# Performance work log

Measured on AMD Instinct MI355X. Metric: run time of the kernel, lower is better.

Reference implementation:

```python
import jax, jax.numpy as jnp
import numpy as np

# Fixed reactor dimensions and grey-box constants (from hyb_greybox_pars / xuyscales)
NX, NU, NY, NP = 3, 1, 2, 4
NZ = NP * (NY + NU)          # 12
F, V, DELTA = 0.1, 1.0, 1.0
CAMEAN, CBMEAN = 1.0, 0.5    # yscale mean
CASTD, CBSTD = 0.5, 0.3      # yscale std
CAFMEAN, CAFSTD = 2.0, 0.5   # uscale


def _fnn(x, layers):
    """Feed-forward NN: tanh hidden layers, linear output layer."""
    for W, b in layers[:-1]:
        x = jnp.tanh(x @ W + b)
    W, b = layers[-1]
    return x @ W + b


def setup_inputs() -> dict:
    key = jax.random.key(0)
    ks = jax.random.split(key, 16)
    B, T = 2048, 1024
    d = {
        "useq": jax.random.normal(ks[0], (B, T, NU), jnp.float32),
        "x0": 0.1 * jax.random.normal(ks[1], (B, NX + NZ), jnp.float32),
    }
    s1 = 1.0 / np.sqrt(1.0)
    s16 = 1.0 / np.sqrt(16.0)
    s12 = 1.0 / np.sqrt(12.0)
    s32 = 1.0 / np.sqrt(32.0)
    for i, name in enumerate(["r1", "r2", "r3"]):
        d[name + "_W0"] = s1 * jax.random.normal(ks[2 + 2 * i], (1, 16), jnp.float32)
        d[name + "_b0"] = jnp.zeros((16,), jnp.float32)
        d[name + "_W1"] = s16 * jax.random.normal(ks[3 + 2 * i], (16, 1), jnp.float32)
        d[name + "_b1"] = jnp.zeros((1,), jnp.float32)
    d["estC_W0"] = s12 * jax.random.normal(ks[10], (12, 32), jnp.float32)
    d["estC_b0"] = jnp.zeros((32,), jnp.float32)
    d["estC_W1"] = s32 * jax.random.normal(ks[11], (32, 1), jnp.float32)
    d["estC_b1"] = jnp.zeros((1,), jnp.float32)
    return d


def reference(useq, x0,
              r1_W0, r1_b0, r1_W1, r1_b1,
              r2_W0, r2_b0, r2_W1, r2_b1,
              r3_W0, r3_b0, r3_W1, r3_b1,
              estC_W0, estC_b0, estC_W1, estC_b1):
    r1L = [(r1_W0, r1_b0), (r1_W1, r1_b1)]
    r2L = [(r2_W0, r2_b0), (r2_W1, r2_b1)]
    r3L = [(r3_W0, r3_b0), (r3_W1, r3_b1)]
    estCL = [(estC_W0, estC_b0), (estC_W1, estC_b1)]

    def fxu(x, u):
        Ca, Cb, Cc = x[:, 0:1], x[:, 1:2], x[:, 2:3]
        Caf = u[:, 0:1]
        r1 = _fnn(Ca, r1L) * CASTD
        r2 = _fnn(Cb, r2L) * CBSTD
        r3 = _fnn(Cc, r3L) * CBSTD
        Ca = Ca * CASTD + CAMEAN
        Cb = Cb * CBSTD + CBMEAN
        Cc = Cc * CBSTD + CBMEAN
        Caf = Caf * CAFSTD + CAFMEAN
        dCa = F * (Caf - Ca) / V - r1
        dCb = -F * Cb / V + r1 - 3.0 * r2 + r3
        dCc = -F * Cc / V + r2 - r3
        return jnp.concatenate([dCa / CASTD, dCb / CBSTD, dCc / CBSTD], axis=-1)

    def step(xz, u):
        x, z = xz[:, :NX], xz[:, NX:]
        ypseq, upseq = z[:, :NP * NY], z[:, NP * NY:]
        k1 = fxu(x, u)
        k2 = fxu(x + DELTA * (k1 / 2.0), u)
        k3 = fxu(x + DELTA * (k2 / 2.0), u)
        k4 = fxu(x + DELTA * k3, u)
        xplus = x + (DELTA / 6.0) * (k1 + 2.0 * k2 + 2.0 * k3 + k4)
        zplus = jnp.concatenate([ypseq[:, NY:], x[:, :NY], upseq[:, NU:], u], axis=-1)
        CcNN = _fnn(z, estCL)
        y = jnp.concatenate([x, CcNN], axis=-1)   # [B, Ny + 2*numUnmeasGb] = [B, 4]
        return jnp.concatenate([xplus, zplus], axis=-1), y

    u_t = jnp.swapaxes(useq, 0, 1)                # [T, B, Nu]
    _, ys = jax.lax.scan(step, x0, u_t)           # ys: [T, B, 4]
    return jnp.swapaxes(ys, 0, 1)                 # [B, T, 4]
```

## Files before the change

### kernel.cpp

```cpp
#include <hip/hip_runtime.h>

#define TT 1024
#define BB 2048
#define K1 8
#define L2E2 2.8853900817779268f

typedef float v2f __attribute__((ext_vector_type(2)));

template <int CTRL>
__device__ __forceinline__ float dpp_add(float x) {
  int y = __builtin_amdgcn_update_dpp(0, __float_as_int(x), CTRL, 0xF, 0xF, true);
  return x + __int_as_float(y);
}
__device__ __forceinline__ float sum16(float x) {
  x = dpp_add<0xB1>(x);
  x = dpp_add<0x4E>(x);
  x = dpp_add<0x141>(x);
  x = dpp_add<0x140>(x);
  return x;
}
__device__ __forceinline__ float rdlane(float x, int l) {
  return __int_as_float(__builtin_amdgcn_readlane(__float_as_int(x), l));
}
__device__ __forceinline__ v2f pkfma(float s, v2f w, v2f a) {
  return __builtin_elementwise_fma((v2f){s, s}, w, a);
}

__global__ __launch_bounds__(256) void phase1_kernel(
    const float* __restrict__ useq, const float* __restrict__ x0,
    const float* __restrict__ r1W0, const float* __restrict__ r1b0,
    const float* __restrict__ r1W1, const float* __restrict__ r1b1,
    const float* __restrict__ r2W0, const float* __restrict__ r2b0,
    const float* __restrict__ r2W1, const float* __restrict__ r2b1,
    const float* __restrict__ r3W0, const float* __restrict__ r3b0,
    const float* __restrict__ r3W1, const float* __restrict__ r3b1,
    float* __restrict__ out) {
  const int lane = threadIdx.x & 63;
  const int row = lane >> 4;
  const int j = lane & 15;
  const int e =
      __builtin_amdgcn_readfirstlane(blockIdx.x * 4 + (threadIdx.x >> 6));

  const float* W0p = (row == 0) ? r1W0 : (row == 1) ? r2W0 : r3W0;
  const float* b0p = (row == 0) ? r1b0 : (row == 1) ? r2b0 : r3b0;
  const float* W1p = (row == 0) ? r1W1 : (row == 1) ? r2W1 : r3W1;

  const float w0s = W0p[j] * L2E2;
  const float b0s = b0p[j] * L2E2;
  const float wn = -2.0f * W1p[j];
  const float iwn = 1.0f / wn;

  float C1 = r1b1[0], C2 = r2b1[0], C3 = r3b1[0];
  for (int q = 0; q < 16; ++q) {
    C1 += r1W1[q];
    C2 += r2W1[q];
    C3 += r3W1[q];
  }
  const float caC = 0.2f - C1;
  const float cbC = -1.0f / 6.0f + (5.0f / 3.0f) * C1 - 3.0f * C2 + C3;
  const float ccC = -1.0f / 6.0f + C2 - C3;

  const float cstBase = (row == 0) ? caC : (row == 1) ? cbC : ccC;
  const float uco = (row == 0) ? 0.1f : 0.0f;
  const float a1 = (row == 0) ? -1.0f : (row == 1) ? (5.0f / 3.0f) : 0.0f;
  const float a2 = (row == 1) ? -3.0f : (row == 2) ? 1.0f : 0.0f;
  const float a3 = (row == 1) ? 1.0f : (row == 2) ? -1.0f : 0.0f;

  float S = x0[e * 15 + ((row < 3) ? row : 2)];

  const float* up = useq + e * TT;
  float* op = out + (size_t)e * TT * 4;

#define STAGE(SS, KK)                                                     \
  {                                                                       \
    float e_ = __builtin_amdgcn_exp2f(fmaf(w0s, (SS), b0s));              \
    float q = sum16(__builtin_amdgcn_rcpf(fmaf(e_, iwn, iwn)));           \
    float P1 = rdlane(q, 0);                                              \
    float P2 = rdlane(q, 16);                                             \
    float P3 = rdlane(q, 32);                                             \
    float t_ = fmaf(-0.1f, (SS), cstS);                                   \
    t_ = fmaf(a1, P1, t_);                                                \
    t_ = fmaf(a2, P2, t_);                                                \
    KK = fmaf(a3, P3, t_);                                                \
  }

#define STEP(UQ, SC_)                                                     \
  {                                                                       \
    const float cstS = fmaf(uco, (UQ), cstBase);                          \
    SC_ = S;                                                              \
    float k1, k2, k3, k4;                                                 \
    STAGE(S, k1)                                                          \
    float s2 = fmaf(0.5f, k1, S);                                         \
    STAGE(s2, k2)                                                         \
    float s3 = fmaf(0.5f, k2, S);                                         \
    STAGE(s3, k3)                                                         \
    float s4 = S + k3;                                                    \
    STAGE(s4, k4)                                                         \
    S = fmaf(1.0f / 6.0f, fmaf(2.0f, k2 + k3, k1) + k4, S);               \
  }

  float uc0, uc1, uc2, uc3, uc4, uc5, uc6, uc7;
  {
    float4 a = *(const float4*)(up);
    float4 b = *(const float4*)(up + 4);
    uc0 = a.x; uc1 = a.y; uc2 = a.z; uc3 = a.w;
    uc4 = b.x; uc5 = b.y; uc6 = b.z; uc7 = b.w;
  }

  for (int t0 = 0; t0 < TT; t0 += K1) {
    const int tn = (t0 + K1 <= TT - K1) ? (t0 + K1) : (TT - K1);
    const float4 na = *(const float4*)(up + tn);
    const float4 nb = *(const float4*)(up + tn + 4);

    float sc0, sc1, sc2, sc3, sc4, sc5, sc6, sc7;
    STEP(uc0, sc0)
    STEP(uc1, sc1)
    STEP(uc2, sc2)
    STEP(uc3, sc3)
    STEP(uc4, sc4)
    STEP(uc5, sc5)
    STEP(uc6, sc6)
    STEP(uc7, sc7)

    if (j == 0 && row < 3) {
      float* p = op + t0 * 4 + row;
      p[0] = sc0;  p[4] = sc1;  p[8] = sc2;  p[12] = sc3;
      p[16] = sc4; p[20] = sc5; p[24] = sc6; p[28] = sc7;
    }

    uc0 = na.x; uc1 = na.y; uc2 = na.z; uc3 = na.w;
    uc4 = nb.x; uc5 = nb.y; uc6 = nb.z; uc7 = nb.w;
  }
#undef STEP
#undef STAGE
}

__global__ __launch_bounds__(256) void phase2_kernel(
    const float* __restrict__ useq, const float* __restrict__ x0,
    const float* __restrict__ W0, const float* __restrict__ b0,
    const float* __restrict__ W1, const float* __restrict__ b1p,
    float* __restrict__ out) {
  __shared__ float4 wq[16][8];
  if (threadIdx.x < 128) {
    const int p = threadIdx.x >> 3, q = threadIdx.x & 7;
    float4 v = {0.0f, 0.0f, 0.0f, 0.0f};
    if (q < 6) {
      v.x = W0[(2 * q) * 32 + 2 * p] * L2E2;
      v.y = W0[(2 * q) * 32 + 2 * p + 1] * L2E2;
      v.z = W0[(2 * q + 1) * 32 + 2 * p] * L2E2;
      v.w = W0[(2 * q + 1) * 32 + 2 * p + 1] * L2E2;
    } else if (q == 6) {
      v.x = b0[2 * p] * L2E2;
      v.y = b0[2 * p + 1] * L2E2;
      v.z = -2.0f * W1[2 * p];
      v.w = -2.0f * W1[2 * p + 1];
    }
    wq[p][q] = v;
  }
  __syncthreads();

  float base = b1p[0];
#pragma unroll
  for (int h = 0; h < 32; ++h) base += W1[h];

  const int b = blockIdx.x * 2 + (threadIdx.x >> 7);
  const int tid = threadIdx.x & 127;
  const float* xrow = x0 + b * 15;

  v2f zy[8][4];
  float zu[8][4];
#pragma unroll
  for (int k = 0; k < 8; ++k) {
    const int t = k * 128 + tid;
    const int g = (b << 10) + t;
    if (t >= 4) {
      const v2f* py = (const v2f*)(out) + (size_t)(g - 4) * 2;
#pragma unroll
      for (int i = 0; i < 4; ++i) zy[k][i] = py[2 * i];
      const float* pu = useq + g - 4;
#pragma unroll
      for (int i = 0; i < 4; ++i) zu[k][i] = pu[i];
    } else {
#pragma unroll
      for (int i = 0; i < 4; ++i) {
        const int s4 = t - 4 + i;
        if (s4 >= 0) {
          const v2f* py = (const v2f*)(out) + (size_t)((b << 10) + s4) * 2;
          zy[k][i] = py[0];
          zu[k][i] = useq[(b << 10) + s4];
        } else {
          zy[k][i] = (v2f){xrow[3 + 2 * (i + t)], xrow[4 + 2 * (i + t)]};
          zu[k][i] = xrow[11 + i + t];
        }
      }
    }
  }

  float ov0 = base, ov1 = base, ov2 = base, ov3 = base;
  float ov4 = base, ov5 = base, ov6 = base, ov7 = base;
#pragma unroll
  for (int p = 0; p < 16; ++p) {
    const float4 w01 = wq[p][0];
    const float4 w23 = wq[p][1];
    const float4 w45 = wq[p][2];
    const float4 w67 = wq[p][3];
    const float4 wu01 = wq[p][4];
    const float4 wu23 = wq[p][5];
    const float4 wb = wq[p][6];
#define ACC2(OV, ZY, ZU)                                                  \
  {                                                                       \
    v2f a = (v2f){wb.x, wb.y};                                            \
    a = pkfma(ZY[0].x, (v2f){w01.x, w01.y}, a);                           \
    a = pkfma(ZY[0].y, (v2f){w01.z, w01.w}, a);                           \
    a = pkfma(ZY[1].x, (v2f){w23.x, w23.y}, a);                           \
    a = pkfma(ZY[1].y, (v2f){w23.z, w23.w}, a);                           \
    a = pkfma(ZY[2].x, (v2f){w45.x, w45.y}, a);                           \
    a = pkfma(ZY[2].y, (v2f){w45.z, w45.w}, a);                           \
    a = pkfma(ZY[3].x, (v2f){w67.x, w67.y}, a);                           \
    a = pkfma(ZY[3].y, (v2f){w67.z, w67.w}, a);                           \
    a = pkfma(ZU[0], (v2f){wu01.x, wu01.y}, a);                           \
    a = pkfma(ZU[1], (v2f){wu01.z, wu01.w}, a);                           \
    a = pkfma(ZU[2], (v2f){wu23.x, wu23.y}, a);                           \
    a = pkfma(ZU[3], (v2f){wu23.z, wu23.w}, a);                           \
    const float sx =                                                      \
        __builtin_amdgcn_rcpf(__builtin_amdgcn_exp2f(a.x) + 1.0f);        \
    const float sy =                                                      \
        __builtin_amdgcn_rcpf(__builtin_amdgcn_exp2f(a.y) + 1.0f);        \
    OV = fmaf(wb.z, sx, OV);                                              \
    OV = fmaf(wb.w, sy, OV);                                              \
  }
    ACC2(ov0, zy[0], zu[0])
    ACC2(ov1, zy[1], zu[1])
    ACC2(ov2, zy[2], zu[2])
    ACC2(ov3, zy[3], zu[3])
    ACC2(ov4, zy[4], zu[4])
    ACC2(ov5, zy[5], zu[5])
    ACC2(ov6, zy[6], zu[6])
    ACC2(ov7, zy[7], zu[7])
#undef ACC2
  }

  const size_t gb = (size_t)(b << 10) + tid;
  out[(gb + 0) * 4 + 3] = ov0;
  out[(gb + 128) * 4 + 3] = ov1;
  out[(gb + 256) * 4 + 3] = ov2;
  out[(gb + 384) * 4 + 3] = ov3;
  out[(gb + 512) * 4 + 3] = ov4;
  out[(gb + 640) * 4 + 3] = ov5;
  out[(gb + 768) * 4 + 3] = ov6;
  out[(gb + 896) * 4 + 3] = ov7;
}

extern "C" void kernel_launch(void* const* d_in, const int* in_sizes, int n_in,
                              void* d_out, int out_size, void* d_ws,
                              size_t ws_size, hipStream_t stream) {
  const float* useq = (const float*)d_in[0];
  const float* x0 = (const float*)d_in[1];
  float* out = (float*)d_out;

  phase1_kernel<<<BB / 4, 256, 0, stream>>>(
      useq, x0,
      (const float*)d_in[2], (const float*)d_in[3], (const float*)d_in[4],
      (const float*)d_in[5], (const float*)d_in[6], (const float*)d_in[7],
      (const float*)d_in[8], (const float*)d_in[9], (const float*)d_in[10],
      (const float*)d_in[11], (const float*)d_in[12], (const float*)d_in[13],
      out);

  phase2_kernel<<<BB / 2, 256, 0, stream>>>(
      useq, x0, (const float*)d_in[14], (const float*)d_in[15],
      (const float*)d_in[16], (const float*)d_in[17], out);
}
```

Baseline: 445.0 us.

## Interleave two batch trajectories per wave in RK4 scan; contiguous time windows in phase2

Phase 1 now has each wavefront integrate two independent batch rows at once, interleaving their exp/rcp/DPP-reduction/readlane chains. The aim is to hide the long serial dependency latency of the per-step recurrence, at the cost of launching half as many blocks. Phase 2 now gives each thread 8 consecutive timesteps and builds them from a shared 11-element sliding window, instead of gathering 4-wide history separately for strided timesteps, which cuts redundant global loads. The lower block count in phase 1 may reduce occupancy across CUs.

```diff
diff --git a/kernel.cpp b/kernel.cpp
--- a/kernel.cpp
+++ b/kernel.cpp
@@ -2,7 +2,6 @@
 
 #define TT 1024
 #define BB 2048
-#define K1 8
 #define L2E2 2.8853900817779268f
 
 typedef float v2f __attribute__((ext_vector_type(2)));
@@ -11,13 +10,6 @@
 __device__ __forceinline__ float dpp_add(float x) {
   int y = __builtin_amdgcn_update_dpp(0, __float_as_int(x), CTRL, 0xF, 0xF, true);
   return x + __int_as_float(y);
-}
-__device__ __forceinline__ float sum16(float x) {
-  x = dpp_add<0xB1>(x);
-  x = dpp_add<0x4E>(x);
-  x = dpp_add<0x141>(x);
-  x = dpp_add<0x140>(x);
-  return x;
 }
 __device__ __forceinline__ float rdlane(float x, int l) {
   return __int_as_float(__builtin_amdgcn_readlane(__float_as_int(x), l));
@@ -38,8 +30,9 @@
   const int lane = threadIdx.x & 63;
   const int row = lane >> 4;
   const int j = lane & 15;
-  const int e =
-      __builtin_amdgcn_readfirstlane(blockIdx.x * 4 + (threadIdx.x >> 6));
+  const int e0 = __builtin_amdgcn_readfirstlane(
+      (blockIdx.x * 4 + (threadIdx.x >> 6)) * 2);
+  const int e1 = e0 + 1;
 
   const float* W0p = (row == 0) ? r1W0 : (row == 1) ? r2W0 : r3W0;
   const float* b0p = (row == 0) ? r1b0 : (row == 1) ? r2b0 : r3b0;
@@ -66,73 +59,81 @@
   const float a2 = (row == 1) ? -3.0f : (row == 2) ? 1.0f : 0.0f;
   const float a3 = (row == 1) ? 1.0f : (row == 2) ? -1.0f : 0.0f;
 
-  float S = x0[e * 15 + ((row < 3) ? row : 2)];
-
-  const float* up = useq + e * TT;
-  float* op = out + (size_t)e * TT * 4;
-
-#define STAGE(SS, KK)                                                     \
+  const int srow = (row < 3) ? row : 2;
+  float S0 = x0[e0 * 15 + srow];
+  float S1 = x0[e1 * 15 + srow];
+
+  const float* up0 = useq + e0 * TT;
+  const float* up1 = useq + e1 * TT;
+  float* op0 = out + (size_t)e0 * TT * 4;
+  float* op1 = out + (size_t)e1 * TT * 4;
+
+#define STAGE2(SA, SB, KA, KB)                                            \
   {                                                                       \
-    float e_ = __builtin_amdgcn_exp2f(fmaf(w0s, (SS), b0s));              \
-    float q = sum16(__builtin_amdgcn_rcpf(fmaf(e_, iwn, iwn)));           \
-    float P1 = rdlane(q, 0);                                              \
-    float P2 = rdlane(q, 16);                                             \
-    float P3 = rdlane(q, 32);                                             \
-    float t_ = fmaf(-0.1f, (SS), cstS);                                   \
-    t_ = fmaf(a1, P1, t_);                                                \
-    t_ = fmaf(a2, P2, t_);                                                \
-    KK = fmaf(a3, P3, t_);                                                \
-  }
-
-#define STEP(UQ, SC_)                                                     \
+    float ea_ = __builtin_amdgcn_exp2f(fmaf(w0s, (SA), b0s));             \
+    float eb_ = __builtin_amdgcn_exp2f(fmaf(w0s, (SB), b0s));             \
+    float qa_ = __builtin_amdgcn_rcpf(fmaf(ea_, iwn, iwn));               \
+    float qb_ = __builtin_amdgcn_rcpf(fmaf(eb_, iwn, iwn));               \
+    qa_ = dpp_add<0xB1>(qa_);   qb_ = dpp_add<0xB1>(qb_);                 \
+    qa_ = dpp_add<0x4E>(qa_);   qb_ = dpp_add<0x4E>(qb_);                 \
+    qa_ = dpp_add<0x141>(qa_);  qb_ = dpp_add<0x141>(qb_);                \
+    qa_ = dpp_add<0x140>(qa_);  qb_ = dpp_add<0x140>(qb_);                \
+    float P1a = rdlane(qa_, 0);                                           \
+    float P1b = rdlane(qb_, 0);                                           \
+    float P2a = rdlane(qa_, 16);                                          \
+    float P2b = rdlane(qb_, 16);                                          \
+    float P3a = rdlane(qa_, 32);                                          \
+    float P3b = rdlane(qb_, 32);                                          \
+    float ta_ = fmaf(-0.1f, (SA), cstSa);                                 \
+    float tb_ = fmaf(-0.1f, (SB), cstSb);                                 \
+    ta_ = fmaf(a1, P1a, ta_);   tb_ = fmaf(a1, P1b, tb_);                 \
+    ta_ = fmaf(a2, P2a, ta_);   tb_ = fmaf(a2, P2b, tb_);                 \
+    KA = fmaf(a3, P3a, ta_);    KB = fmaf(a3, P3b, tb_);                  \
+  }
+
+#define STEP2(UA, UB, SCA, SCB)                                           \
   {                                                                       \
-    const float cstS = fmaf(uco, (UQ), cstBase);                          \
-    SC_ = S;                                                              \
-    float k1, k2, k3, k4;                                                 \
-    STAGE(S, k1)                                                          \
-    float s2 = fmaf(0.5f, k1, S);                                         \
-    STAGE(s2, k2)                                                         \
-    float s3 = fmaf(0.5f, k2, S);                                         \
-    STAGE(s3, k3)                                                         \
-    float s4 = S + k3;                                                    \
-    STAGE(s4, k4)                                                         \
-    S = fmaf(1.0f / 6.0f, fmaf(2.0f, k2 + k3, k1) + k4, S);               \
-  }
-
-  float uc0, uc1, uc2, uc3, uc4, uc5, uc6, uc7;
-  {
-    float4 a = *(const float4*)(up);
-    float4 b = *(const float4*)(up + 4);
-    uc0 = a.x; uc1 = a.y; uc2 = a.z; uc3 = a.w;
-    uc4 = b.x; uc5 = b.y; uc6 = b.z; uc7 = b.w;
-  }
-
-  for (int t0 = 0; t0 < TT; t0 += K1) {
-    const int tn = (t0 + K1 <= TT - K1) ? (t0 + K1) : (TT - K1);
-    const float4 na = *(const float4*)(up + tn);
-    const float4 nb = *(const float4*)(up + tn + 4);
-
-    float sc0, sc1, sc2, sc3, sc4, sc5, sc6, sc7;
-    STEP(uc0, sc0)
-    STEP(uc1, sc1)
-    STEP(uc2, sc2)
-    STEP(uc3, sc3)
-    STEP(uc4, sc4)
-    STEP(uc5, sc5)
-    STEP(uc6, sc6)
-    STEP(uc7, sc7)
+    const float cstSa = fmaf(uco, (UA), cstBase);                         \
+    const float cstSb = fmaf(uco, (UB), cstBase);                         \
+    SCA = S0;  SCB = S1;                                                  \
+    float k1a, k2a, k3a, k4a, k1b, k2b, k3b, k4b;                         \
+    STAGE2(S0, S1, k1a, k1b)                                              \
+    float s2a = fmaf(0.5f, k1a, S0), s2b = fmaf(0.5f, k1b, S1);           \
+    STAGE2(s2a, s2b, k2a, k2b)                                            \
+    float s3a = fmaf(0.5f, k2a, S0), s3b = fmaf(0.5f, k2b, S1);           \
+    STAGE2(s3a, s3b, k3a, k3b)                                            \
+    float s4a = S0 + k3a, s4b = S1 + k3b;                                 \
+    STAGE2(s4a, s4b, k4a, k4b)                                            \
+    S0 = fmaf(1.0f / 6.0f, fmaf(2.0f, k2a + k3a, k1a) + k4a, S0);         \
+    S1 = fmaf(1.0f / 6.0f, fmaf(2.0f, k2b + k3b, k1b) + k4b, S1);         \
+  }
+
+  float4 cura = *(const float4*)(up0);
+  float4 curb = *(const float4*)(up1);
+
+  for (int t0 = 0; t0 < TT; t0 += 4) {
+    const int tn = (t0 + 4 <= TT - 4) ? (t0 + 4) : (TT - 4);
+    const float4 naa = *(const float4*)(up0 + tn);
+    const float4 nab = *(const float4*)(up1 + tn);
+
+    float sa0, sa1, sa2, sa3, sb0, sb1, sb2, sb3;
+    STEP2(cura.x, curb.x, sa0, sb0)
+    STEP2(cura.y, curb.y, sa1, sb1)
+    STEP2(cura.z, curb.z, sa2, sb2)
+    STEP2(cura.w, curb.w, sa3, sb3)
 
     if (j == 0 && row < 3) {
-      float* p = op + t0 * 4 + row;
-      p[0] = sc0;  p[4] = sc1;  p[8] = sc2;  p[12] = sc3;
-      p[16] = sc4; p[20] = sc5; p[24] = sc6; p[28] = sc7;
-    }
-
-    uc0 = na.x; uc1 = na.y; uc2 = na.z; uc3 = na.w;
-    uc4 = nb.x; uc5 = nb.y; uc6 = nb.z; uc7 = nb.w;
-  }
-#undef STEP
-#undef STAGE
+      float* pa = op0 + t0 * 4 + row;
+      pa[0] = sa0;  pa[4] = sa1;  pa[8] = sa2;  pa[12] = sa3;
+      float* pb = op1 + t0 * 4 + row;
+      pb[0] = sb0;  pb[4] = sb1;  pb[8] = sb2;  pb[12] = sb3;
+    }
+
+    cura = naa;
+    curb = nab;
+  }
+#undef STEP2
+#undef STAGE2
 }
 
 __global__ __launch_bounds__(256) void phase2_kernel(
@@ -165,39 +166,41 @@
 
   const int b = blockIdx.x * 2 + (threadIdx.x >> 7);
   const int tid = threadIdx.x & 127;
+  const int t0 = tid * 8;
   const float* xrow = x0 + b * 15;
 
-  v2f zy[8][4];
-  float zu[8][4];
-#pragma unroll
-  for (int k = 0; k < 8; ++k) {
-    const int t = k * 128 + tid;
-    const int g = (b << 10) + t;
-    if (t >= 4) {
-      const v2f* py = (const v2f*)(out) + (size_t)(g - 4) * 2;
-#pragma unroll
-      for (int i = 0; i < 4; ++i) zy[k][i] = py[2 * i];
-      const float* pu = useq + g - 4;
-#pragma unroll
-      for (int i = 0; i < 4; ++i) zu[k][i] = pu[i];
-    } else {
-#pragma unroll
-      for (int i = 0; i < 4; ++i) {
-        const int s4 = t - 4 + i;
-        if (s4 >= 0) {
-          const v2f* py = (const v2f*)(out) + (size_t)((b << 10) + s4) * 2;
-          zy[k][i] = py[0];
-          zu[k][i] = useq[(b << 10) + s4];
-        } else {
-          zy[k][i] = (v2f){xrow[3 + 2 * (i + t)], xrow[4 + 2 * (i + t)]};
-          zu[k][i] = xrow[11 + i + t];
-        }
-      }
-    }
-  }
-
-  float ov0 = base, ov1 = base, ov2 = base, ov3 = base;
-  float ov4 = base, ov5 = base, ov6 = base, ov7 = base;
+  v2f hy[11];
+  float hu[11];
+  if (tid != 0) {
+    const float* py = out + ((size_t)(b << 10) + t0 - 4) * 4;
+#pragma unroll
+    for (int i = 0; i < 11; ++i) hy[i] = *(const v2f*)(py + i * 4);
+    const float* pu = useq + (b << 10) + t0 - 4;
+    const float4 ua = *(const float4*)(pu);
+    const float4 ub = *(const float4*)(pu + 4);
+    const float4 uc = *(const float4*)(pu + 8);
+    hu[0] = ua.x; hu[1] = ua.y; hu[2] = ua.z; hu[3] = ua.w;
+    hu[4] = ub.x; hu[5] = ub.y; hu[6] = ub.z; hu[7] = ub.w;
+    hu[8] = uc.x; hu[9] = uc.y; hu[10] = uc.z;
+  } else {
+#pragma unroll
+    for (int i = 0; i < 4; ++i) {
+      hy[i] = (v2f){xrow[3 + 2 * i], xrow[4 + 2 * i]};
+      hu[i] = xrow[11 + i];
+    }
+    const float* py = out + ((size_t)(b << 10)) * 4;
+    const float* pu = useq + (b << 10);
+#pragma unroll
+    for (int i = 4; i < 11; ++i) {
+      hy[i] = *(const v2f*)(py + (i - 4) * 4);
+      hu[i] = pu[i - 4];
+    }
+  }
+
+  float ov[8];
+#pragma unroll
+  for (int k = 0; k < 8; ++k) ov[k] = base;
+
 #pragma unroll
   for (int p = 0; p < 16; ++p) {
     const float4 w01 = wq[p][0];
@@ -210,18 +213,18 @@
 #define ACC2(OV, ZY, ZU)                                                  \
   {                                                                       \
     v2f a = (v2f){wb.x, wb.y};                                            \
-    a = pkfma(ZY[0].x, (v2f){w01.x, w01.y}, a);                           \
-    a = pkfma(ZY[0].y, (v2f){w01.z, w01.w}, a);                           \
-    a = pkfma(ZY[1].x, (v2f){w23.x, w23.y}, a);                           \
-    a = pkfma(ZY[1].y, (v2f){w23.z, w23.w}, a);                           \
-    a = pkfma(ZY[2].x, (v2f){w45.x, w45.y}, a);                           \
-    a = pkfma(ZY[2].y, (v2f){w45.z, w45.w}, a);                           \
-    a = pkfma(ZY[3].x, (v2f){w67.x, w67.y}, a);                           \
-    a = pkfma(ZY[3].y, (v2f){w67.z, w67.w}, a);                           \
-    a = pkfma(ZU[0], (v2f){wu01.x, wu01.y}, a);                           \
-    a = pkfma(ZU[1], (v2f){wu01.z, wu01.w}, a);                           \
-    a = pkfma(ZU[2], (v2f){wu23.x, wu23.y}, a);                           \
-    a = pkfma(ZU[3], (v2f){wu23.z, wu23.w}, a);                           \
+    a = pkfma((ZY)[0].x, (v2f){w01.x, w01.y}, a);                         \
+    a = pkfma((ZY)[0].y, (v2f){w01.z, w01.w}, a);                         \
+    a = pkfma((ZY)[1].x, (v2f){w23.x, w23.y}, a);                         \
+    a = pkfma((ZY)[1].y, (v2f){w23.z, w23.w}, a);                         \
+    a = pkfma((ZY)[2].x, (v2f){w45.x, w45.y}, a);                         \
+    a = pkfma((ZY)[2].y, (v2f){w45.z, w45.w}, a);                         \
+    a = pkfma((ZY)[3].x, (v2f){w67.x, w67.y}, a);                         \
+    a = pkfma((ZY)[3].y, (v2f){w67.z, w67.w}, a);                         \
+    a = pkfma((ZU)[0], (v2f){wu01.x, wu01.y}, a);                         \
+    a = pkfma((ZU)[1], (v2f){wu01.z, wu01.w}, a);                         \
+    a = pkfma((ZU)[2], (v2f){wu23.x, wu23.y}, a);                         \
+    a = pkfma((ZU)[3], (v2f){wu23.z, wu23.w}, a);                         \
     const float sx =                                                      \
         __builtin_amdgcn_rcpf(__builtin_amdgcn_exp2f(a.x) + 1.0f);        \
     const float sy =                                                      \
@@ -229,26 +232,14 @@
     OV = fmaf(wb.z, sx, OV);                                              \
     OV = fmaf(wb.w, sy, OV);                                              \
   }
-    ACC2(ov0, zy[0], zu[0])
-    ACC2(ov1, zy[1], zu[1])
-    ACC2(ov2, zy[2], zu[2])
-    ACC2(ov3, zy[3], zu[3])
-    ACC2(ov4, zy[4], zu[4])
-    ACC2(ov5, zy[5], zu[5])
-    ACC2(ov6, zy[6], zu[6])
-    ACC2(ov7, zy[7], zu[7])
+#pragma unroll
+    for (int k = 0; k < 8; ++k) ACC2(ov[k], (&hy[k]), (&hu[k]))
 #undef ACC2
   }
 
-  const size_t gb = (size_t)(b << 10) + tid;
-  out[(gb + 0) * 4 + 3] = ov0;
-  out[(gb + 128) * 4 + 3] = ov1;
-  out[(gb + 256) * 4 + 3] = ov2;
-  out[(gb + 384) * 4 + 3] = ov3;
-  out[(gb + 512) * 4 + 3] = ov4;
-  out[(gb + 640) * 4 + 3] = ov5;
-  out[(gb + 768) * 4 + 3] = ov6;
-  out[(gb + 896) * 4 + 3] = ov7;
+  float* po = out + ((size_t)(b << 10) + t0) * 4 + 3;
+#pragma unroll
+  for (int k = 0; k < 8; ++k) po[4 * k] = ov[k];
 }
 
 extern "C" void kernel_launch(void* const* d_in, const int* in_sizes, int n_in,
@@ -258,7 +249,7 @@
   const float* x0 = (const float*)d_in[1];
   float* out = (float*)d_out;
 
-  phase1_kernel<<<BB / 4, 256, 0, stream>>>(
+  phase1_kernel<<<BB / 8, 256, 0, stream>>>(
       useq, x0,
       (const float*)d_in[2], (const float*)d_in[3], (const float*)d_in[4],
       (const float*)d_in[5], (const float*)d_in[6], (const float*)d_in[7],
```

Result: no change. 444.3 us (-0.2%).
